# Optimization experiments

Measured on AMD Instinct MI355X. Metric: run time of the kernel, lower is better.

## Reference

```python
import jax, jax.numpy as jnp
import numpy as np

EPS = 1e-12      # LayerNorm eps in Selector
TAU = 1e-6       # gumbel-softmax temperature
TOPK = 2         # seg_selector.topk
TOPJ = 128       # reg_selector.topk
NUMC, NUMF_PER_C, NUMP, DIM, QDIM = 4, 4, 256, 1024, 512


def _ln(x, g, b):
    m = x.mean(-1, keepdims=True)
    v = ((x - m) ** 2).mean(-1, keepdims=True)
    return (x - m) / jnp.sqrt(v + EPS) * g + b


def _selector(q, K, V_flat, Wq, bq, ln_q_g, ln_q_b, Wk, bk, ln_k_g, ln_k_b, topk, key):
    # q: (B, qdim); K: (B, n, dim); V_flat: (B, n, F)
    Qp = _ln(q @ Wq.T + bq, ln_q_g, ln_q_b)                      # (B, dim)
    Kp = _ln(K @ Wk.T + bk, ln_k_g, ln_k_b)                      # (B, n, dim)
    probs = jax.nn.softmax(jnp.einsum('bnd,bd->bn', Kp, Qp), axis=-1)  # (B, n)
    B, n = probs.shape
    # F.gumbel_softmax applied to the softmax probs (as in the torch code),
    # vectorized over the topk loop: one mask per selection round.
    u = jax.random.uniform(key, (B, topk, n), minval=1e-20, maxval=1.0)
    g = -jnp.log(-jnp.log(u))
    masks = jax.nn.softmax((probs[:, None, :] + g) / TAU, axis=-1)     # (B, topk, n)
    return jnp.einsum('btn,bnf->btf', masks, V_flat)                   # (B, topk, F)


def setup_inputs() -> dict:
    key = jax.random.key(0)
    ks = jax.random.split(key, 24)
    bz = 8
    s = 0.02
    d = {
        'q_feat': jax.random.normal(ks[0], (bz, QDIM, 1), dtype=jnp.float32),
        'image_embeds': jax.random.normal(ks[1], (bz, NUMC, NUMF_PER_C, NUMP, DIM), dtype=jnp.float32),
        'video_cls': jax.random.normal(ks[2], (bz, NUMC * NUMF_PER_C, DIM), dtype=jnp.float32),
        # seg_selector params
        'seg_Wq': s * jax.random.normal(ks[3], (DIM, QDIM), dtype=jnp.float32),
        'seg_bq': jnp.zeros((DIM,), jnp.float32),
        'seg_ln_q_g': jnp.ones((DIM,), jnp.float32),
        'seg_ln_q_b': jnp.zeros((DIM,), jnp.float32),
        'seg_Wk': s * jax.random.normal(ks[4], (DIM, DIM), dtype=jnp.float32),
        'seg_bk': jnp.zeros((DIM,), jnp.float32),
        'seg_ln_k_g': jnp.ones((DIM,), jnp.float32),
        'seg_ln_k_b': jnp.zeros((DIM,), jnp.float32),
        # reg_selector params
        'reg_Wq': s * jax.random.normal(ks[5], (DIM, QDIM), dtype=jnp.float32),
        'reg_bq': jnp.zeros((DIM,), jnp.float32),
        'reg_ln_q_g': jnp.ones((DIM,), jnp.float32),
        'reg_ln_q_b': jnp.zeros((DIM,), jnp.float32),
        'reg_Wk': s * jax.random.normal(ks[6], (DIM, DIM), dtype=jnp.float32),
        'reg_bk': jnp.zeros((DIM,), jnp.float32),
        'reg_ln_k_g': jnp.ones((DIM,), jnp.float32),
        'reg_ln_k_b': jnp.zeros((DIM,), jnp.float32),
    }
    return d


def reference(q_feat, image_embeds, video_cls,
              seg_Wq, seg_bq, seg_ln_q_g, seg_ln_q_b, seg_Wk, seg_bk, seg_ln_k_g, seg_ln_k_b,
              reg_Wq, reg_bq, reg_ln_q_g, reg_ln_q_b, reg_Wk, reg_bk, reg_ln_k_g, reg_ln_k_b):
    bz = q_feat.shape[0]
    # video_in.view(bz, numc*numf, nump, -1); hdim == dim so no projections
    video_feat = image_embeds.reshape(bz, NUMC * NUMF_PER_C, NUMP, DIM)
    vc = video_cls / jnp.linalg.norm(video_cls, axis=-1, keepdims=True)
    seg_feat = vc.reshape(bz, NUMC, NUMF_PER_C, DIM).mean(axis=2)        # (bz, numc, dim)
    # CLIP text feature, L2-normalized (get_clip_txt_embedding)
    q = q_feat[..., 0]
    q = q / jnp.linalg.norm(q, axis=-1, keepdims=True)                   # (bz, qdim)

    k1, k2 = jax.random.split(jax.random.key(42))
    # seg_selector: K=seg_feat (bz,4,dim), V=video_feat viewed (bz,4, 4*256*1024)
    sel = _selector(q, seg_feat, video_feat.reshape(bz, NUMC, -1),
                    seg_Wq, seg_bq, seg_ln_q_g, seg_ln_q_b,
                    seg_Wk, seg_bk, seg_ln_k_g, seg_ln_k_b, TOPK, k1)
    sel = sel.reshape(bz, TOPK * NUMF_PER_C, NUMP, DIM)                  # (bz, 8, 256, 1024)

    # reg_selector over the flattened pseudo-batch (bz*8)
    B2 = bz * TOPK * NUMF_PER_C
    K2 = sel.reshape(B2, NUMP, DIM)
    q2 = jnp.repeat(q, TOPK * NUMF_PER_C, axis=0)                        # (bz*8, qdim)
    sel2 = _selector(q2, K2, K2, reg_Wq, reg_bq, reg_ln_q_g, reg_ln_q_b,
                     reg_Wk, reg_bk, reg_ln_k_g, reg_ln_k_b, TOPJ, k2)   # (bz*8, 128, 1024)

    return sel2.reshape(bz, 1, TOPK * NUMF_PER_C, TOPJ, DIM)
```

## Files before the change

### kernel.cpp

```cpp
#include <hip/hip_runtime.h>
#include <hip/hip_fp16.h>
#include <stdint.h>

#ifndef JAX_PARTITIONABLE
#define JAX_PARTITIONABLE 1
#endif

typedef _Float16 f16x8 __attribute__((ext_vector_type(8)));
typedef float    f32x4 __attribute__((ext_vector_type(4)));

static constexpr int BZ   = 8;
static constexpr int QD   = 512;
static constexpr int DIM  = 1024;
static constexpr int I2   = 64;
static constexpr int TOPJ = 128;
static constexpr int NROW = 16384;
static constexpr int NCT  = 4;

static constexpr size_t EAI = 0;
static constexpr size_t EWI = (size_t)33554432;
static constexpr size_t FQN   = 17825792;
static constexpr size_t FSF   = FQN + 4096;
static constexpr size_t FYS   = FSF + 32768;
static constexpr size_t FYR   = FYS + 8192;
static constexpr size_t FY2   = FYR + 8192;
static constexpr size_t FGQ   = FY2 + 32768;
static constexpr size_t FSG   = FGQ + 8192;
static constexpr size_t FCL   = FSG + 8;
static constexpr size_t FMS   = FCL + 8;
static constexpr size_t FP2   = FMS + 64;
static constexpr size_t FPART = FP2 + 16384;

__device__ __forceinline__ uint32_t rotl32(uint32_t v, int d){ return (v << d) | (v >> (32 - d)); }

__device__ __forceinline__ void tf2x32(uint32_t k0, uint32_t k1, uint32_t x0, uint32_t x1,
                                       uint32_t& o0, uint32_t& o1){
  const uint32_t ks2 = k0 ^ k1 ^ 0x1BD11BDAu;
  x0 += k0; x1 += k1;
#define TFR(r) x0 += x1; x1 = rotl32(x1, r); x1 ^= x0;
  TFR(13) TFR(15) TFR(26) TFR(6)
  x0 += k1;  x1 += ks2 + 1u;
  TFR(17) TFR(29) TFR(16) TFR(24)
  x0 += ks2; x1 += k0 + 2u;
  TFR(13) TFR(15) TFR(26) TFR(6)
  x0 += k0;  x1 += k1 + 3u;
  TFR(17) TFR(29) TFR(16) TFR(24)
  x0 += k1;  x1 += ks2 + 4u;
  TFR(13) TFR(15) TFR(26) TFR(6)
  x0 += ks2; x1 += k0 + 5u;
#undef TFR
  o0 = x0; o1 = x1;
}

__device__ __forceinline__ void jax_keys(uint32_t& k1a, uint32_t& k1b, uint32_t& k2a, uint32_t& k2b){
#if JAX_PARTITIONABLE
  uint32_t a,b,c,d;
  tf2x32(0u, 42u, 0u, 0u, a, b);
  tf2x32(0u, 42u, 0u, 1u, c, d);
  k1a = a; k1b = b; k2a = c; k2b = d;
#else
  uint32_t a,b,c,d;
  tf2x32(0u, 42u, 0u, 2u, a, b);
  tf2x32(0u, 42u, 1u, 3u, c, d);
  k1a = a; k1b = c; k2a = b; k2b = d;
#endif
}

__device__ __forceinline__ float jax_uniform(uint32_t ka, uint32_t kb, uint32_t idx, uint32_t half_n){
  uint32_t o0, o1, bits;
#if JAX_PARTITIONABLE
  (void)half_n;
  tf2x32(ka, kb, 0u, idx, o0, o1);
  bits = o0 ^ o1;
#else
  if (idx < half_n){ tf2x32(ka, kb, idx, idx + half_n, o0, o1); bits = o0; }
  else             { tf2x32(ka, kb, idx - half_n, idx, o0, o1); bits = o1; }
#endif
  float f = __uint_as_float((bits >> 9) | 0x3f800000u) - 1.0f;
  f = f + 1e-20f;
  return fmaxf(f, 1e-20f);
}

__device__ __forceinline__ float blk_sum(float v, float* red){
  __syncthreads();
  #pragma unroll
  for (int m = 32; m >= 1; m >>= 1) v += __shfl_xor(v, m);
  if ((threadIdx.x & 63) == 0) red[threadIdx.x >> 6] = v;
  __syncthreads();
  return red[0] + red[1] + red[2] + red[3];
}
__device__ __forceinline__ float blk_max(float v, float* red){
  __syncthreads();
  #pragma unroll
  for (int m = 32; m >= 1; m >>= 1) v = fmaxf(v, __shfl_xor(v, m));
  if ((threadIdx.x & 63) == 0) red[threadIdx.x >> 6] = v;
  __syncthreads();
  return fmaxf(fmaxf(red[0], red[1]), fmaxf(red[2], red[3]));
}

__device__ __forceinline__ unsigned short f2h(float x){
  return __half_as_ushort(__float2half(x));
}
__device__ __forceinline__ float h2f(unsigned short u){
  return __half2float(__ushort_as_half(u));
}

__device__ __forceinline__ void gl_lds16(const void* g, void* l){
  __builtin_amdgcn_global_load_lds((const __attribute__((address_space(1))) void*)g,
                                   (__attribute__((address_space(3))) void*)l, 16, 0, 0);
}

__global__ __launch_bounds__(256) void k_norm(const float* __restrict__ qf,
                                              const float* __restrict__ vcls,
                                              float* __restrict__ ws)
{
  const int b = blockIdx.x, tid = threadIdx.x;
  __shared__ float red[4];
  float q0 = qf[b * QD + tid];
  float q1 = qf[b * QD + 256 + tid];
  float ss = blk_sum(q0*q0 + q1*q1, red);
  float nrm = sqrtf(ss);
  ws[FQN + (size_t)b * QD + tid]       = q0 / nrm;
  ws[FQN + (size_t)b * QD + 256 + tid] = q1 / nrm;

  float sf[4][4];
  #pragma unroll
  for (int c = 0; c < 4; ++c)
    #pragma unroll
    for (int r = 0; r < 4; ++r) sf[c][r] = 0.f;

  for (int f = 0; f < 16; ++f){
    float v[4]; float s2 = 0.f;
    #pragma unroll
    for (int r = 0; r < 4; ++r){
      v[r] = vcls[((size_t)(b * 16 + f)) * DIM + tid + (r << 8)];
      s2 += v[r] * v[r];
    }
    float s = blk_sum(s2, red);
    float n2 = sqrtf(s);
    const int c = f >> 2;
    #pragma unroll
    for (int r = 0; r < 4; ++r) sf[c][r] += v[r] / n2;
  }
  #pragma unroll
  for (int c = 0; c < 4; ++c)
    #pragma unroll
    for (int r = 0; r < 4; ++r)
      ws[FSF + ((size_t)(b * 4 + c)) * DIM + tid + (r << 8)] = sf[c][r] * 0.25f;
}

__global__ __launch_bounds__(256) void k_matvec(
    const float* __restrict__ sWq, const float* __restrict__ sbq,
    const float* __restrict__ rWq, const float* __restrict__ rbq,
    const float* __restrict__ sWk, const float* __restrict__ sbk,
    float* __restrict__ ws)
{
  const int bid = blockIdx.x;
  const int b = bid >> 5, ch = bid & 31;
  const int tid = threadIdx.x;
  const int di = tid >> 3, sub = tid & 7;
  const int d = ch * 32 + di;
  const float* qn = ws + FQN + (size_t)b * QD;
  const float* sf = ws + FSF + (size_t)b * 4 * DIM;

  {
    const float* wr = sWq + (size_t)d * QD + sub * 64;
    const float* qq = qn + sub * 64;
    float a = 0.f;
    #pragma unroll
    for (int e = 0; e < 64; e += 4){
      float4 w4 = *(const float4*)(wr + e);
      a += qq[e]*w4.x + qq[e+1]*w4.y + qq[e+2]*w4.z + qq[e+3]*w4.w;
    }
    a += __shfl_xor(a, 1); a += __shfl_xor(a, 2); a += __shfl_xor(a, 4);
    if (sub == 0) ws[FYS + (size_t)b * DIM + d] = a + sbq[d];
  }
  {
    const float* wr = rWq + (size_t)d * QD + sub * 64;
    const float* qq = qn + sub * 64;
    float a = 0.f;
    #pragma unroll
    for (int e = 0; e < 64; e += 4){
      float4 w4 = *(const float4*)(wr + e);
      a += qq[e]*w4.x + qq[e+1]*w4.y + qq[e+2]*w4.z + qq[e+3]*w4.w;
    }
    a += __shfl_xor(a, 1); a += __shfl_xor(a, 2); a += __shfl_xor(a, 4);
    if (sub == 0) ws[FYR + (size_t)b * DIM + d] = a + rbq[d];
  }
  for (int c = 0; c < 4; ++c){
    const float* wr = sWk + (size_t)d * DIM + sub * 128;
    const float* qq = sf + (size_t)c * DIM + sub * 128;
    float a = 0.f;
    #pragma unroll
    for (int e = 0; e < 128; e += 4){
      float4 w4 = *(const float4*)(wr + e);
      a += qq[e]*w4.x + qq[e+1]*w4.y + qq[e+2]*w4.z + qq[e+3]*w4.w;
    }
    a += __shfl_xor(a, 1); a += __shfl_xor(a, 2); a += __shfl_xor(a, 4);
    if (sub == 0) ws[FY2 + ((size_t)(b * 4 + c)) * DIM + d] = a + sbk[d];
  }
}

__global__ __launch_bounds__(256) void k_post(
    const float* __restrict__ slnqg, const float* __restrict__ slnqb,
    const float* __restrict__ rlnqg, const float* __restrict__ rlnqb,
    const float* __restrict__ rlnkg, const float* __restrict__ rlnkb,
    const float* __restrict__ slnkg, const float* __restrict__ slnkb,
    float* __restrict__ ws)
{
  const int b = blockIdx.x, tid = threadIdx.x;
  __shared__ float red[4];
  __shared__ float qps[DIM];
  __shared__ float lg[4];

  {
    float y[4];
    #pragma unroll
    for (int r = 0; r < 4; ++r) y[r] = ws[FYS + (size_t)b * DIM + tid + (r << 8)];
    float S = blk_sum(y[0]+y[1]+y[2]+y[3], red);
    float mu = S * (1.f / 1024.f);
    float pv = 0.f;
    #pragma unroll
    for (int r = 0; r < 4; ++r){ float dv = y[r]-mu; pv += dv*dv; }
    float V = blk_sum(pv, red);
    float sig = sqrtf(V * (1.f / 1024.f) + 1e-12f);
    #pragma unroll
    for (int r = 0; r < 4; ++r){
      const int d = tid + (r << 8);
      qps[d] = (y[r]-mu)/sig * slnqg[d] + slnqb[d];
    }
  }
  __syncthreads();

  {
    float y[4];
    #pragma unroll
    for (int r = 0; r < 4; ++r) y[r] = ws[FYR + (size_t)b * DIM + tid + (r << 8)];
    float S = blk_sum(y[0]+y[1]+y[2]+y[3], red);
    float mu = S * (1.f / 1024.f);
    float pv = 0.f;
    #pragma unroll
    for (int r = 0; r < 4; ++r){ float dv = y[r]-mu; pv += dv*dv; }
    float V = blk_sum(pv, red);
    float sig = sqrtf(V * (1.f / 1024.f) + 1e-12f);
    float sg = 0.f, cl = 0.f;
    #pragma unroll
    for (int r = 0; r < 4; ++r){
      const int d = tid + (r << 8);
      float o = (y[r]-mu)/sig * rlnqg[d] + rlnqb[d];
      float gv = rlnkg[d] * o;
      ws[FGQ + (size_t)b * DIM + d] = gv;
      sg += gv;
      cl += rlnkb[d] * o;
    }
    float SG = blk_sum(sg, red);
    float CL = blk_sum(cl, red);
    if (tid == 0){ ws[FSG + b] = SG; ws[FCL + b] = CL; }
  }

  for (int c = 0; c < 4; ++c){
    float y[4];
    #pragma unroll
    for (int r = 0; r < 4; ++r) y[r] = ws[FY2 + ((size_t)(b * 4 + c)) * DIM + tid + (r << 8)];
    float S = blk_sum(y[0]+y[1]+y[2]+y[3], red);
    float mu = S * (1.f / 1024.f);
    float pv = 0.f;
    #pragma unroll
    for (int r = 0; r < 4; ++r){ float dv = y[r]-mu; pv += dv*dv; }
    float V = blk_sum(pv, red);
    float sig = sqrtf(V * (1.f / 1024.f) + 1e-12f);
    float lp = 0.f;
    #pragma unroll
    for (int r = 0; r < 4; ++r){
      const int d = tid + (r << 8);
      float kp = (y[r]-mu)/sig * slnkg[d] + slnkb[d];
      lp += kp * qps[d];
    }
    float L = blk_sum(lp, red);
    if (tid == 0) lg[c] = L;
  }
  __syncthreads();

  if (tid == 0){
    float m = fmaxf(fmaxf(lg[0], lg[1]), fmaxf(lg[2], lg[3]));
    float e[4], s = 0.f;
    #pragma unroll
    for (int c = 0; c < 4; ++c){ e[c] = expf(lg[c] - m); s += e[c]; }
    float probs[4];
    #pragma unroll
    for (int c = 0; c < 4; ++c) probs[c] = e[c] / s;
    uint32_t k1a, k1b, k2a, k2b;
    jax_keys(k1a, k1b, k2a, k2b);
    for (int t = 0; t < 2; ++t){
      float x[4];
      #pragma unroll
      for (int c = 0; c < 4; ++c){
        float u = jax_uniform(k1a, k1b, (uint32_t)(b * 8 + t * 4 + c), 32u);
        float gmb = -logf(-logf(u));
        x[c] = (probs[c] + gmb) / 1e-6f;
      }
      float xm = fmaxf(fmaxf(x[0], x[1]), fmaxf(x[2], x[3]));
      float w[4], sw = 0.f;
      #pragma unroll
      for (int c = 0; c < 4; ++c){ w[c] = expf(x[c] - xm); sw += w[c]; }
      #pragma unroll
      for (int c = 0; c < 4; ++c) ws[FMS + b * 8 + t * 4 + c] = w[c] / sw;
    }
  }
}

__global__ __launch_bounds__(256) void k_sel(const float* __restrict__ E,
                                             const float* __restrict__ W,
                                             float* __restrict__ ws)
{
  const int blk = blockIdx.x;
  const int th = threadIdx.x;
  const int kc = th >> 3;
  const int c  = (th & 7) >> 1;
  const int pos = (th & 1) * 4;
  const int d = th << 2;

  if (blk < 2048){
    const int r0 = blk * 8;
    const int i = r0 >> 8;
    const int bz = i >> 3, it = i & 7, t = it >> 2, j = it & 3;
    const int p0 = r0 & 255;
    const float* msk = ws + FMS + bz * 8 + t * 4;

    float4 a[8];
    #pragma unroll
    for (int r = 0; r < 8; ++r) a[r] = (float4){0.f, 0.f, 0.f, 0.f};

    #pragma unroll
    for (int cc = 0; cc < 4; ++cc){
      const float w = msk[cc];
      if (w != 0.f){
        const float* ep = E + (((size_t)((bz * 4 + cc) * 4 + j)) * 256 + p0) * DIM + d;
        #pragma unroll
        for (int r = 0; r < 8; ++r){
          const float4 v = *(const float4*)(ep + (size_t)r * DIM);
          a[r].x = fmaf(w, v.x, a[r].x);
          a[r].y = fmaf(w, v.y, a[r].y);
          a[r].z = fmaf(w, v.z, a[r].z);
          a[r].w = fmaf(w, v.w, a[r].w);
        }
      }
    }
    unsigned short* AI = (unsigned short*)ws + EAI;
    #pragma unroll
    for (int r = 0; r < 8; ++r){
      ushort4 h, l;
      h.x = f2h(a[r].x); l.x = f2h(a[r].x - h2f(h.x));
      h.y = f2h(a[r].y); l.y = f2h(a[r].y - h2f(h.y));
      h.z = f2h(a[r].z); l.z = f2h(a[r].z - h2f(h.z));
      h.w = f2h(a[r].w); l.w = f2h(a[r].w - h2f(h.w));
      const size_t base = (size_t)(r0 + r) * 2048 + kc * 64;
      *(ushort4*)&AI[base + c * 8 + pos]      = h;
      *(ushort4*)&AI[base + c * 8 + pos + 32] = l;
    }
  } else {
    const int r0 = (blk - 2048) * 8;
    unsigned short* WI = (unsigned short*)ws + EWI;
    float4 v[8];
    #pragma unroll
    for (int r = 0; r < 8; ++r)
      v[r] = *(const float4*)&W[(size_t)(r0 + r) * DIM + d];
    #pragma unroll
    for (int r = 0; r < 8; ++r){
      ushort4 h, l;
      h.x = f2h(v[r].x); l.x = f2h(v[r].x - h2f(h.x));
      h.y = f2h(v[r].y); l.y = f2h(v[r].y - h2f(h.y));
      h.z = f2h(v[r].z); l.z = f2h(v[r].z - h2f(h.z));
      h.w = f2h(v[r].w); l.w = f2h(v[r].w - h2f(h.w));
      const size_t base = (size_t)(r0 + r) * 2048 + kc * 64;
      *(ushort4*)&WI[base + c * 8 + pos]      = h;
      *(ushort4*)&WI[base + c * 8 + pos + 32] = l;
    }
  }
}

__global__ __launch_bounds__(512) void k_gemm(const float* __restrict__ bk,
                                              float* __restrict__ ws)
{
  const unsigned short* AI = (const unsigned short*)ws + EAI;
  const unsigned short* WI = (const unsigned short*)ws + EWI;
  const float* gq = ws + FGQ;
  float* part = ws + FPART;

  __shared__ __align__(16) unsigned short Abuf[2][16384];
  __shared__ __align__(16) unsigned short Bbuf[2][16384];

  const int bid = blockIdx.x;
  const int xcd = bid & 7, g = bid >> 3;
  const int rt = xcd * 8 + (g >> 2);
  const int ct = g & 3;
  const int R0 = rt * 256, C0 = ct * 256;
  const int tid = threadIdx.x;
  const int lane = tid & 63, wid = tid >> 6;
  const int wr = wid >> 2, wc = wid & 3;
  const int b = R0 >> 11;

  const int src_off = (lane >> 3) * 2048 + (((lane & 7) ^ (lane >> 3)) << 3);
  const int pcH = ((lane >> 4) ^ (lane & 7)) * 16;
  const int pcL = pcH ^ 64;
  const int raw = wr * 128 + (lane & 15);
  const int rbw = wc * 64 + (lane & 15);

  f32x4 acc[8][4];
  #pragma unroll
  for (int m = 0; m < 8; ++m)
    #pragma unroll
    for (int n = 0; n < 4; ++n)
      acc[m][n] = (f32x4){0.f, 0.f, 0.f, 0.f};

  auto stageA = [&](int buf, int kc){
    const unsigned short* As = AI + (size_t)(R0 + wid * 32) * 2048 + kc * 64 + src_off;
    unsigned short* Ad = &Abuf[buf][wid * 2048];
    #pragma unroll
    for (int q = 0; q < 4; ++q) gl_lds16(As + (size_t)q * 8 * 2048, Ad + q * 512);
  };
  auto stageB = [&](int buf, int kc){
    const unsigned short* Bs = WI + (size_t)(C0 + wid * 32) * 2048 + kc * 64 + src_off;
    unsigned short* Bd = &Bbuf[buf][wid * 2048];
    #pragma unroll
    for (int q = 0; q < 4; ++q) gl_lds16(Bs + (size_t)q * 8 * 2048, Bd + q * 512);
  };

  stageA(0, 0);
  stageB(0, 0);
  asm volatile("s_waitcnt vmcnt(0)" ::: "memory");
  __builtin_amdgcn_s_barrier();

  f16x8 ah[4], al[4], bh[4], bl[4];

  #pragma unroll 1
  for (int kc = 0; kc < 32; ++kc){
    const int cur = kc & 1;
    const char* pa = (const char*)&Abuf[cur][0];
    const char* pb = (const char*)&Bbuf[cur][0];

    #pragma unroll
    for (int f = 0; f < 4; ++f){
      const int ro = (raw + f * 16) << 7;
      ah[f] = *(const f16x8*)(pa + ro + pcH);
      al[f] = *(const f16x8*)(pa + ro + pcL);
    }
    #pragma unroll
    for (int f = 0; f < 2; ++f){
      const int ro = (rbw + f * 16) << 7;
      bh[f] = *(const f16x8*)(pb + ro + pcH);
      bl[f] = *(const f16x8*)(pb + ro + pcL);
    }
    if (kc < 31) stageA(cur ^ 1, kc + 1);
    __builtin_amdgcn_s_barrier();
    asm volatile("s_waitcnt lgkmcnt(0)" ::: "memory");
    __builtin_amdgcn_sched_barrier(0);
    __builtin_amdgcn_s_setprio(1);
    #pragma unroll
    for (int m = 0; m < 4; ++m)
      #pragma unroll
      for (int n = 0; n < 2; ++n){
        acc[m][n] = __builtin_amdgcn_mfma_f32_16x16x32_f16(ah[m], bh[n], acc[m][n], 0, 0, 0);
        acc[m][n] = __builtin_amdgcn_mfma_f32_16x16x32_f16(ah[m], bl[n], acc[m][n], 0, 0, 0);
        acc[m][n] = __builtin_amdgcn_mfma_f32_16x16x32_f16(al[m], bh[n], acc[m][n], 0, 0, 0);
      }
    __builtin_amdgcn_s_setprio(0);
    __builtin_amdgcn_s_barrier();

    #pragma unroll
    for (int f = 2; f < 4; ++f){
      const int ro = (rbw + f * 16) << 7;
      bh[f] = *(const f16x8*)(pb + ro + pcH);
      bl[f] = *(const f16x8*)(pb + ro + pcL);
    }
    if (kc < 31) stageB(cur ^ 1, kc + 1);
    __builtin_amdgcn_s_barrier();
    asm volatile("s_waitcnt lgkmcnt(0)" ::: "memory");
    __builtin_amdgcn_sched_barrier(0);
    __builtin_amdgcn_s_setprio(1);
    #pragma unroll
    for (int m = 0; m < 4; ++m)
      #pragma unroll
      for (int n = 2; n < 4; ++n){
        acc[m][n] = __builtin_amdgcn_mfma_f32_16x16x32_f16(ah[m], bh[n], acc[m][n], 0, 0, 0);
        acc[m][n] = __builtin_amdgcn_mfma_f32_16x16x32_f16(ah[m], bl[n], acc[m][n], 0, 0, 0);
        acc[m][n] = __builtin_amdgcn_mfma_f32_16x16x32_f16(al[m], bh[n], acc[m][n], 0, 0, 0);
      }
    __builtin_amdgcn_s_setprio(0);
    __builtin_amdgcn_s_barrier();

    #pragma unroll
    for (int f = 0; f < 4; ++f){
      const int ro = (raw + 64 + f * 16) << 7;
      ah[f] = *(const f16x8*)(pa + ro + pcH);
      al[f] = *(const f16x8*)(pa + ro + pcL);
    }
    __builtin_amdgcn_s_barrier();
    asm volatile("s_waitcnt lgkmcnt(0)" ::: "memory");
    __builtin_amdgcn_sched_barrier(0);
    __builtin_amdgcn_s_setprio(1);
    #pragma unroll
    for (int m = 0; m < 4; ++m)
      #pragma unroll
      for (int n = 0; n < 2; ++n){
        acc[m + 4][n] = __builtin_amdgcn_mfma_f32_16x16x32_f16(ah[m], bh[n], acc[m + 4][n], 0, 0, 0);
        acc[m + 4][n] = __builtin_amdgcn_mfma_f32_16x16x32_f16(ah[m], bl[n], acc[m + 4][n], 0, 0, 0);
        acc[m + 4][n] = __builtin_amdgcn_mfma_f32_16x16x32_f16(al[m], bh[n], acc[m + 4][n], 0, 0, 0);
      }
    __builtin_amdgcn_s_setprio(0);
    __builtin_amdgcn_s_barrier();

    __builtin_amdgcn_s_setprio(1);
    #pragma unroll
    for (int m = 0; m < 4; ++m)
      #pragma unroll
      for (int n = 2; n < 4; ++n){
        acc[m + 4][n] = __builtin_amdgcn_mfma_f32_16x16x32_f16(ah[m], bh[n], acc[m + 4][n], 0, 0, 0);
        acc[m + 4][n] = __builtin_amdgcn_mfma_f32_16x16x32_f16(ah[m], bl[n], acc[m + 4][n], 0, 0, 0);
        acc[m + 4][n] = __builtin_amdgcn_mfma_f32_16x16x32_f16(al[m], bh[n], acc[m + 4][n], 0, 0, 0);
      }
    __builtin_amdgcn_s_setprio(0);
    asm volatile("s_waitcnt vmcnt(0)" ::: "memory");
    __builtin_amdgcn_sched_barrier(0);
    __builtin_amdgcn_s_barrier();
  }

  float bkv[4], gv[4];
  #pragma unroll
  for (int n = 0; n < 4; ++n){
    const int col = C0 + wc * 64 + n * 16 + (lane & 15);
    bkv[n] = bk[col];
    gv[n]  = gq[(size_t)b * DIM + col];
  }
  float* fred = (float*)&Abuf[0][0];
  #pragma unroll
  for (int m = 0; m < 8; ++m)
    #pragma unroll
    for (int r = 0; r < 4; ++r){
      float s = 0.f, q = 0.f, tv = 0.f;
      #pragma unroll
      for (int n = 0; n < 4; ++n){
        float y = acc[m][n][r] + bkv[n];
        s += y; q += y * y; tv += y * gv[n];
      }
      #pragma unroll
      for (int msk = 8; msk >= 1; msk >>= 1){
        s += __shfl_xor(s, msk); q += __shfl_xor(q, msk); tv += __shfl_xor(tv, msk);
      }
      if ((lane & 15) == 0){
        const int rl = wr * 128 + m * 16 + (lane >> 4) * 4 + r;
        fred[(rl * 4 + wc) * 3 + 0] = s;
        fred[(rl * 4 + wc) * 3 + 1] = q;
        fred[(rl * 4 + wc) * 3 + 2] = tv;
      }
    }
  __syncthreads();
  if (tid < 256){
    #pragma unroll
    for (int st = 0; st < 3; ++st){
      float v = fred[(tid * 4 + 0) * 3 + st] + fred[(tid * 4 + 1) * 3 + st]
              + fred[(tid * 4 + 2) * 3 + st] + fred[(tid * 4 + 3) * 3 + st];
      part[((size_t)ct * NROW + R0 + tid) * 3 + st] = v;
    }
  }
}

__global__ __launch_bounds__(256) void k_probs2(float* __restrict__ ws)
{
  const int i = blockIdx.x, tid = threadIdx.x;
  const int r = i * 256 + tid;
  const int b = i >> 3;
  __shared__ float red[4];
  const float* part = ws + FPART;
  float S = 0.f, Q = 0.f, T = 0.f;
  #pragma unroll
  for (int ct = 0; ct < NCT; ++ct){
    const float* pp = part + ((size_t)ct * NROW + r) * 3;
    S += pp[0]; Q += pp[1]; T += pp[2];
  }
  float mu  = S * (1.f / 1024.f);
  float var = Q * (1.f / 1024.f) - mu * mu;
  float sig = sqrtf(var + 1e-12f);
  float L = (T - mu * ws[FSG + b]) / sig + ws[FCL + b];
  float M = blk_max(L, red);
  float w = expf(L - M);
  float sw = blk_sum(w, red);
  ws[FP2 + r] = w / sw;
}

__global__ __launch_bounds__(256) void k_out(const float* __restrict__ E,
                                             const float* __restrict__ ws,
                                             float* __restrict__ out)
{
  const int bid = blockIdx.x;
  const int i = bid >> 7, t2 = bid & 127;
  const int bz = i >> 3, it = i & 7, tt = it >> 2, j = it & 3;
  const int tid = threadIdx.x;
  __shared__ float red[4];
  __shared__ float wv[256];
  __shared__ float mloc[4];
  __shared__ unsigned long long mk[4];

  if (tid < 4) mloc[tid] = ws[FMS + bz * 8 + tt * 4 + tid];

  uint32_t k1a, k1b, k2a, k2b;
  jax_keys(k1a, k1b, k2a, k2b);
  const uint32_t fidx = ((uint32_t)(i * TOPJ + t2)) * 256u + (uint32_t)tid;
  float u = jax_uniform(k2a, k2b, fidx, 1048576u);
  float gmb = -logf(-logf(u));
  float x = (ws[FP2 + (size_t)i * 256 + tid] + gmb) / 1e-6f;
  float M = blk_max(x, red);
  float w = expf(x - M);
  float sw = blk_sum(w, red);
  float wn = w / sw;
  wv[tid] = wn;
  unsigned long long bal = __ballot(wn != 0.f);
  if ((tid & 63) == 0) mk[tid >> 6] = bal;
  __syncthreads();

  const int d = tid << 2;
  float4 acc = {0.f, 0.f, 0.f, 0.f};
  for (int wq = 0; wq < 4; ++wq){
    unsigned long long mm = mk[wq];
    while (mm){
      const int l = __ffsll(mm) - 1;
      mm &= mm - 1;
      const int p = (wq << 6) + l;
      const float wp = wv[p];
      #pragma unroll
      for (int c = 0; c < 4; ++c){
        const float mc = mloc[c];
        if (mc != 0.f){
          const float4 v = *(const float4*)&E[(((size_t)((bz * 4 + c) * 4 + j)) * 256 + p) * DIM + d];
          const float wm = wp * mc;
          acc.x += wm * v.x; acc.y += wm * v.y; acc.z += wm * v.z; acc.w += wm * v.w;
        }
      }
    }
  }
  *(float4*)&out[((size_t)(i * TOPJ + t2)) * DIM + d] = acc;
}

extern "C" void kernel_launch(void* const* d_in, const int* in_sizes, int n_in,
                              void* d_out, int out_size, void* d_ws, size_t ws_size,
                              hipStream_t stream)
{
  const float* qf    = (const float*)d_in[0];
  const float* E     = (const float*)d_in[1];
  const float* vcls  = (const float*)d_in[2];
  const float* sWq   = (const float*)d_in[3];
  const float* sbq   = (const float*)d_in[4];
  const float* slnqg = (const float*)d_in[5];
  const float* slnqb = (const float*)d_in[6];
  const float* sWk   = (const float*)d_in[7];
  const float* sbk   = (const float*)d_in[8];
  const float* slnkg = (const float*)d_in[9];
  const float* slnkb = (const float*)d_in[10];
  const float* rWq   = (const float*)d_in[11];
  const float* rbq   = (const float*)d_in[12];
  const float* rlnqg = (const float*)d_in[13];
  const float* rlnqb = (const float*)d_in[14];
  const float* rWk   = (const float*)d_in[15];
  const float* rbk   = (const float*)d_in[16];
  const float* rlnkg = (const float*)d_in[17];
  const float* rlnkb = (const float*)d_in[18];
  float* ws  = (float*)d_ws;
  float* out = (float*)d_out;

  k_norm<<<BZ, 256, 0, stream>>>(qf, vcls, ws);
  k_matvec<<<256, 256, 0, stream>>>(sWq, sbq, rWq, rbq, sWk, sbk, ws);
  k_post<<<BZ, 256, 0, stream>>>(slnqg, slnqb, rlnqg, rlnqb, rlnkg, rlnkb, slnkg, slnkb, ws);
  k_sel<<<2176, 256, 0, stream>>>(E, rWk, ws);
  k_gemm<<<256, 512, 0, stream>>>(rbk, ws);
  k_probs2<<<I2, 256, 0, stream>>>(ws);
  k_out<<<I2 * TOPJ, 256, 0, stream>>>(E, ws, out);
}
```

Baseline: 177.9 us.

## Fuse norm into matvec, probs2 into output, and trim GEMM barriers

Removes the k_norm kernel by having each k_matvec block recompute the query and segment-feature normalisation into shared memory. It also removes k_probs2 by recomputing the reg-selector softmax inside each k_out block, and drops the intermediate s_barriers in the GEMM main loop. The aim is to cut two kernel launches and some barrier stalls. In exchange the normalisation work is repeated 32 times per batch and the softmax 128 times per row. Removing barriers around the double-buffered LDS staging risks races between the staging writes and other waves' reads.

```diff
diff --git a/kernel.cpp b/kernel.cpp
--- a/kernel.cpp
+++ b/kernel.cpp
@@ -110,46 +110,8 @@
                                    (__attribute__((address_space(3))) void*)l, 16, 0, 0);
 }
 
-__global__ __launch_bounds__(256) void k_norm(const float* __restrict__ qf,
-                                              const float* __restrict__ vcls,
-                                              float* __restrict__ ws)
-{
-  const int b = blockIdx.x, tid = threadIdx.x;
-  __shared__ float red[4];
-  float q0 = qf[b * QD + tid];
-  float q1 = qf[b * QD + 256 + tid];
-  float ss = blk_sum(q0*q0 + q1*q1, red);
-  float nrm = sqrtf(ss);
-  ws[FQN + (size_t)b * QD + tid]       = q0 / nrm;
-  ws[FQN + (size_t)b * QD + 256 + tid] = q1 / nrm;
-
-  float sf[4][4];
-  #pragma unroll
-  for (int c = 0; c < 4; ++c)
-    #pragma unroll
-    for (int r = 0; r < 4; ++r) sf[c][r] = 0.f;
-
-  for (int f = 0; f < 16; ++f){
-    float v[4]; float s2 = 0.f;
-    #pragma unroll
-    for (int r = 0; r < 4; ++r){
-      v[r] = vcls[((size_t)(b * 16 + f)) * DIM + tid + (r << 8)];
-      s2 += v[r] * v[r];
-    }
-    float s = blk_sum(s2, red);
-    float n2 = sqrtf(s);
-    const int c = f >> 2;
-    #pragma unroll
-    for (int r = 0; r < 4; ++r) sf[c][r] += v[r] / n2;
-  }
-  #pragma unroll
-  for (int c = 0; c < 4; ++c)
-    #pragma unroll
-    for (int r = 0; r < 4; ++r)
-      ws[FSF + ((size_t)(b * 4 + c)) * DIM + tid + (r << 8)] = sf[c][r] * 0.25f;
-}
-
 __global__ __launch_bounds__(256) void k_matvec(
+    const float* __restrict__ qf, const float* __restrict__ vcls,
     const float* __restrict__ sWq, const float* __restrict__ sbq,
     const float* __restrict__ rWq, const float* __restrict__ rbq,
     const float* __restrict__ sWk, const float* __restrict__ sbk,
@@ -158,10 +120,47 @@
   const int bid = blockIdx.x;
   const int b = bid >> 5, ch = bid & 31;
   const int tid = threadIdx.x;
+  __shared__ float red[4];
+  __shared__ float qn[QD];
+  __shared__ float sf[4][DIM];
+
+  {
+    float q0 = qf[b * QD + tid];
+    float q1 = qf[b * QD + 256 + tid];
+    float ss = blk_sum(q0*q0 + q1*q1, red);
+    float nrm = sqrtf(ss);
+    qn[tid] = q0 / nrm;
+    qn[tid + 256] = q1 / nrm;
+  }
+  {
+    float sfr[4][4];
+    #pragma unroll
+    for (int c = 0; c < 4; ++c)
+      #pragma unroll
+      for (int r = 0; r < 4; ++r) sfr[c][r] = 0.f;
+    for (int f = 0; f < 16; ++f){
+      float v[4]; float s2 = 0.f;
+      #pragma unroll
+      for (int r = 0; r < 4; ++r){
+        v[r] = vcls[((size_t)(b * 16 + f)) * DIM + tid + (r << 8)];
+        s2 += v[r] * v[r];
+      }
+      float s = blk_sum(s2, red);
+      float n2 = sqrtf(s);
+      const int c = f >> 2;
+      #pragma unroll
+      for (int r = 0; r < 4; ++r) sfr[c][r] += v[r] / n2;
+    }
+    #pragma unroll
+    for (int c = 0; c < 4; ++c)
+      #pragma unroll
+      for (int r = 0; r < 4; ++r)
+        sf[c][tid + (r << 8)] = sfr[c][r] * 0.25f;
+  }
+  __syncthreads();
+
   const int di = tid >> 3, sub = tid & 7;
   const int d = ch * 32 + di;
-  const float* qn = ws + FQN + (size_t)b * QD;
-  const float* sf = ws + FSF + (size_t)b * 4 * DIM;
 
   {
     const float* wr = sWq + (size_t)d * QD + sub * 64;
@@ -189,7 +188,7 @@
   }
   for (int c = 0; c < 4; ++c){
     const float* wr = sWk + (size_t)d * DIM + sub * 128;
-    const float* qq = sf + (size_t)c * DIM + sub * 128;
+    const float* qq = &sf[c][sub * 128];
     float a = 0.f;
     #pragma unroll
     for (int e = 0; e < 128; e += 4){
@@ -452,7 +451,6 @@
       bl[f] = *(const f16x8*)(pb + ro + pcL);
     }
     if (kc < 31) stageA(cur ^ 1, kc + 1);
-    __builtin_amdgcn_s_barrier();
     asm volatile("s_waitcnt lgkmcnt(0)" ::: "memory");
     __builtin_amdgcn_sched_barrier(0);
     __builtin_amdgcn_s_setprio(1);
@@ -465,7 +463,6 @@
         acc[m][n] = __builtin_amdgcn_mfma_f32_16x16x32_f16(al[m], bh[n], acc[m][n], 0, 0, 0);
       }
     __builtin_amdgcn_s_setprio(0);
-    __builtin_amdgcn_s_barrier();
 
     #pragma unroll
     for (int f = 2; f < 4; ++f){
@@ -474,7 +471,6 @@
       bl[f] = *(const f16x8*)(pb + ro + pcL);
     }
     if (kc < 31) stageB(cur ^ 1, kc + 1);
-    __builtin_amdgcn_s_barrier();
     asm volatile("s_waitcnt lgkmcnt(0)" ::: "memory");
     __builtin_amdgcn_sched_barrier(0);
     __builtin_amdgcn_s_setprio(1);
@@ -487,7 +483,6 @@
         acc[m][n] = __builtin_amdgcn_mfma_f32_16x16x32_f16(al[m], bh[n], acc[m][n], 0, 0, 0);
       }
     __builtin_amdgcn_s_setprio(0);
-    __builtin_amdgcn_s_barrier();
 
     #pragma unroll
     for (int f = 0; f < 4; ++f){
@@ -495,7 +490,6 @@
       ah[f] = *(const f16x8*)(pa + ro + pcH);
       al[f] = *(const f16x8*)(pa + ro + pcL);
     }
-    __builtin_amdgcn_s_barrier();
     asm volatile("s_waitcnt lgkmcnt(0)" ::: "memory");
     __builtin_amdgcn_sched_barrier(0);
     __builtin_amdgcn_s_setprio(1);
@@ -508,7 +502,6 @@
         acc[m + 4][n] = __builtin_amdgcn_mfma_f32_16x16x32_f16(al[m], bh[n], acc[m + 4][n], 0, 0, 0);
       }
     __builtin_amdgcn_s_setprio(0);
-    __builtin_amdgcn_s_barrier();
 
     __builtin_amdgcn_s_setprio(1);
     #pragma unroll
@@ -520,8 +513,9 @@
         acc[m + 4][n] = __builtin_amdgcn_mfma_f32_16x16x32_f16(al[m], bh[n], acc[m + 4][n], 0, 0, 0);
       }
     __builtin_amdgcn_s_setprio(0);
+    asm volatile("s_waitcnt lgkmcnt(0)" ::: "memory");
+    __builtin_amdgcn_sched_barrier(0);
     asm volatile("s_waitcnt vmcnt(0)" ::: "memory");
-    __builtin_amdgcn_sched_barrier(0);
     __builtin_amdgcn_s_barrier();
   }
 
@@ -563,29 +557,6 @@
       part[((size_t)ct * NROW + R0 + tid) * 3 + st] = v;
     }
   }
-}
-
-__global__ __launch_bounds__(256) void k_probs2(float* __restrict__ ws)
-{
-  const int i = blockIdx.x, tid = threadIdx.x;
-  const int r = i * 256 + tid;
-  const int b = i >> 3;
-  __shared__ float red[4];
-  const float* part = ws + FPART;
-  float S = 0.f, Q = 0.f, T = 0.f;
-  #pragma unroll
-  for (int ct = 0; ct < NCT; ++ct){
-    const float* pp = part + ((size_t)ct * NROW + r) * 3;
-    S += pp[0]; Q += pp[1]; T += pp[2];
-  }
-  float mu  = S * (1.f / 1024.f);
-  float var = Q * (1.f / 1024.f) - mu * mu;
-  float sig = sqrtf(var + 1e-12f);
-  float L = (T - mu * ws[FSG + b]) / sig + ws[FCL + b];
-  float M = blk_max(L, red);
-  float w = expf(L - M);
-  float sw = blk_sum(w, red);
-  ws[FP2 + r] = w / sw;
 }
 
 __global__ __launch_bounds__(256) void k_out(const float* __restrict__ E,
@@ -603,12 +574,29 @@
 
   if (tid < 4) mloc[tid] = ws[FMS + bz * 8 + tt * 4 + tid];
 
+  const float* part = ws + FPART;
+  const int r = i * 256 + tid;
+  float S = 0.f, Q = 0.f, T = 0.f;
+  #pragma unroll
+  for (int ct = 0; ct < NCT; ++ct){
+    const float* pp = part + ((size_t)ct * NROW + r) * 3;
+    S += pp[0]; Q += pp[1]; T += pp[2];
+  }
+  float mu  = S * (1.f / 1024.f);
+  float var = Q * (1.f / 1024.f) - mu * mu;
+  float sig = sqrtf(var + 1e-12f);
+  float L = (T - mu * ws[FSG + bz]) / sig + ws[FCL + bz];
+  float ML = blk_max(L, red);
+  float wp2 = expf(L - ML);
+  float swp = blk_sum(wp2, red);
+  float p2 = wp2 / swp;
+
   uint32_t k1a, k1b, k2a, k2b;
   jax_keys(k1a, k1b, k2a, k2b);
   const uint32_t fidx = ((uint32_t)(i * TOPJ + t2)) * 256u + (uint32_t)tid;
   float u = jax_uniform(k2a, k2b, fidx, 1048576u);
   float gmb = -logf(-logf(u));
-  float x = (ws[FP2 + (size_t)i * 256 + tid] + gmb) / 1e-6f;
+  float x = (p2 + gmb) / 1e-6f;
   float M = blk_max(x, red);
   float w = expf(x - M);
   float sw = blk_sum(w, red);
@@ -626,13 +614,13 @@
       const int l = __ffsll(mm) - 1;
       mm &= mm - 1;
       const int p = (wq << 6) + l;
-      const float wp = wv[p];
+      const float wpv = wv[p];
       #pragma unroll
       for (int c = 0; c < 4; ++c){
         const float mc = mloc[c];
         if (mc != 0.f){
           const float4 v = *(const float4*)&E[(((size_t)((bz * 4 + c) * 4 + j)) * 256 + p) * DIM + d];
-          const float wm = wp * mc;
+          const float wm = wpv * mc;
           acc.x += wm * v.x; acc.y += wm * v.y; acc.z += wm * v.z; acc.w += wm * v.w;
         }
       }
@@ -667,11 +655,9 @@
   float* ws  = (float*)d_ws;
   float* out = (float*)d_out;
 
-  k_norm<<<BZ, 256, 0, stream>>>(qf, vcls, ws);
-  k_matvec<<<256, 256, 0, stream>>>(sWq, sbq, rWq, rbq, sWk, sbk, ws);
+  k_matvec<<<256, 256, 0, stream>>>(qf, vcls, sWq, sbq, rWq, rbq, sWk, sbk, ws);
   k_post<<<BZ, 256, 0, stream>>>(slnqg, slnqb, rlnqg, rlnqb, rlnkg, rlnkb, slnkg, slnkb, ws);
   k_sel<<<2176, 256, 0, stream>>>(E, rWk, ws);
   k_gemm<<<256, 512, 0, stream>>>(rbk, ws);
-  k_probs2<<<I2, 256, 0, stream>>>(ws);
   k_out<<<I2 * TOPJ, 256, 0, stream>>>(E, ws, out);
 }
```

After: 164.4 us. -7.6%, faster.
